# Kernel tuning notes

Hardware: AMD Instinct MI355X
Metric: run time of the kernel (lower is better)

## Reference

```python
import jax, jax.numpy as jnp
import numpy as np

LEAK = 0.01  # torch LeakyReLU default negative_slope

def lrelu(x):
    return jnp.where(x >= 0, x, LEAK * x)

def edge_conv(x, src, dst, ea, W1, b1, W2, b2):
    # message: cat(x_i=target, x_j=source, edge_attr) -> Linear -> LeakyReLU -> Linear
    m = jnp.concatenate([x[dst], x[src], ea], axis=1)          # [E, 2F+Fe]
    h = lrelu(m @ W1 + b1) @ W2 + b2                            # [E, H]
    n = x.shape[0]
    agg = jnp.full((n, h.shape[1]), jnp.inf, h.dtype).at[dst].min(h)  # scatter-min at target
    return jnp.where(jnp.isfinite(agg), agg, jnp.zeros_like(agg))     # empty nodes -> 0


def setup_inputs() -> dict:
    key = jax.random.key(0)
    ks = jax.random.split(key, 20)
    B, N, E = 4, 20000, 640000
    NF, AD, EF, H = 2, 1, 1, 8
    inp = {
        "node_features": jax.random.randint(ks[0], (B, N, NF), 0, 10, dtype=jnp.int32),
        "actions": jax.random.normal(ks[1], (B, N), dtype=jnp.float32),
        "edge_index": jax.random.randint(ks[2], (B, 2, E), 0, N, dtype=jnp.int64),
        "edge_features": jax.random.normal(ks[3], (B, E, EF), dtype=jnp.float32),
    }
    d0 = NF + AD  # 3
    def lin(k, fin, fout):
        s = 1.0 / np.sqrt(fin)
        k1, k2 = jax.random.split(k)
        return (jax.random.uniform(k1, (fin, fout), jnp.float32, -s, s),
                jax.random.uniform(k2, (fout,), jnp.float32, -s, s))
    inp["c1_W1"], inp["c1_b1"] = lin(ks[4], 2 * d0 + EF, H)
    inp["c1_W2"], inp["c1_b2"] = lin(ks[5], H, H)
    inp["c2_W1"], inp["c2_b1"] = lin(ks[6], 2 * H + 1, H)
    inp["c2_W2"], inp["c2_b2"] = lin(ks[7], H, H)
    inp["c3_W1"], inp["c3_b1"] = lin(ks[8], 2 * H + 1, H)
    inp["c3_W2"], inp["c3_b2"] = lin(ks[9], H, H)
    inp["lin_W"], inp["lin_b"] = lin(ks[10], d0 + H, 1)
    return inp


def reference(node_features, actions, edge_index, edge_features,
              c1_W1, c1_b1, c1_W2, c1_b2,
              c2_W1, c2_b1, c2_W2, c2_b2,
              c3_W1, c3_b1, c3_W2, c3_b2,
              lin_W, lin_b):
    # x = int(node_features) concat actions  -> float
    x0 = jnp.concatenate([node_features.astype(jnp.int32).astype(jnp.float32),
                          actions[..., None]], axis=-1)  # [B,N,3]

    def per_graph(x0g, eig, eag):
        src, dst = eig[0], eig[1]  # flow source_to_target: x_j=src, x_i=dst
        h = lrelu(edge_conv(x0g, src, dst, eag, c1_W1, c1_b1, c1_W2, c1_b2))
        h = lrelu(edge_conv(h, src, dst, eag, c2_W1, c2_b1, c2_W2, c2_b2))
        h = lrelu(edge_conv(h, src, dst, eag, c3_W1, c3_b1, c3_W2, c3_b2))
        xc = jnp.concatenate([x0g, h], axis=1)  # [N, 3+8]
        return jnp.sum(xc, axis=0)              # sum-pool over nodes

    pooled = jax.vmap(per_graph)(x0, edge_index, edge_features)  # [B, 11]
    return pooled @ lin_W + lin_b  # [B, 1]
```

## Files before the change

### kernel.cpp

```cpp
#include <hip/hip_runtime.h>
#include <hip/hip_cooperative_groups.h>

#define LEAK 0.01f
#define BS 128
#define PCHUNK 4096
#define PT 512
#define CT 512
#define MAXNB 256
#define CPGMAX 256
#define BARSTRIDE 64

__device__ __forceinline__ float lrelu(float v) {
    return v >= 0.f ? v : LEAK * v;
}

__device__ __forceinline__ unsigned int fmin_encode(float x) {
    unsigned int u = __float_as_uint(x);
    return (u & 0x80000000u) ? ~u : (u | 0x80000000u);
}
__device__ __forceinline__ float fmin_decode(unsigned int k) {
    unsigned int u = (k & 0x80000000u) ? (k ^ 0x80000000u) : ~k;
    return __uint_as_float(u);
}

__device__ __forceinline__ unsigned int bf16_rne(float f) {
    unsigned int u = __float_as_uint(f);
    return (u + 0x7FFFu + ((u >> 16) & 1u)) >> 16;
}

__device__ __forceinline__ void block_add(float c, float* dst) {
    __shared__ float wsum[8];
#pragma unroll
    for (int off = 32; off > 0; off >>= 1) c += __shfl_down(c, off, 64);
    int lane = threadIdx.x & 63;
    int wave = threadIdx.x >> 6;
    if (lane == 0) wsum[wave] = c;
    __syncthreads();
    if (threadIdx.x == 0) {
        float s = 0.f;
        int nw = blockDim.x >> 6;
        for (int w = 0; w < nw; ++w) s += wsum[w];
        atomicAdd(dst, s);
    }
}

__device__ __forceinline__ void graph_barrier(int* bar, int target) {
    __syncthreads();
    if (threadIdx.x == 0) {
        __threadfence();
        __hip_atomic_fetch_add(bar, 1, __ATOMIC_RELEASE, __HIP_MEMORY_SCOPE_AGENT);
        while (__hip_atomic_load(bar, __ATOMIC_RELAXED, __HIP_MEMORY_SCOPE_AGENT) <
               target)
            __builtin_amdgcn_s_sleep(2);
        __threadfence();
    }
    __syncthreads();
}


__device__ __forceinline__ void init_body(
    const int* __restrict__ nf, const float* __restrict__ act,
    const float* __restrict__ W1, const float* __restrict__ b1,
    const float* __restrict__ lw, const float* __restrict__ lb,
    float* __restrict__ a1, unsigned short* __restrict__ a2,
    float* __restrict__ out, int N, int b, int ib) {
    int t = threadIdx.x;
    int n = ib * PT + t;
    float c = 0.f;
    if (n < N) {
        size_t i = (size_t)b * N + n;
        float x0 = (float)nf[i * 2 + 0];
        float x1 = (float)nf[i * 2 + 1];
        float x2 = act[i];
        float v1[8], v2[8];
#pragma unroll
        for (int j = 0; j < 8; ++j) {
            v1[j] = b1[j] + x0 * W1[0 * 8 + j] + x1 * W1[1 * 8 + j] + x2 * W1[2 * 8 + j];
            v2[j] =         x0 * W1[3 * 8 + j] + x1 * W1[4 * 8 + j] + x2 * W1[5 * 8 + j];
        }
        float4* o1 = (float4*)(a1 + i * 8);
        o1[0] = make_float4(v1[0], v1[1], v1[2], v1[3]);
        o1[1] = make_float4(v1[4], v1[5], v1[6], v1[7]);
        unsigned int w[4];
#pragma unroll
        for (int q = 0; q < 4; ++q)
            w[q] = bf16_rne(v2[2 * q]) | (bf16_rne(v2[2 * q + 1]) << 16);
        *(int4*)(a2 + i * 8) = make_int4(w[0], w[1], w[2], w[3]);
        c = x0 * lw[0] + x1 * lw[1] + x2 * lw[2];
        if (n == 0) c += lb[0];
    }
    block_add(c, &out[b]);
}

__device__ __forceinline__ void part_body(
    const int* __restrict__ ei, const float* __restrict__ ea,
    int2* __restrict__ pairs, int* __restrict__ ofs,
    int E, int NB, int CPG, int b, int c,
    int* __restrict__ lc, int* __restrict__ lofs, int* __restrict__ ts) {
    int t = threadIdx.x;
    for (int i = t; i < NB; i += PT) lc[i] = 0;
    __syncthreads();

    int e0 = c * PCHUNK;
    int end = min(e0 + PCHUNK, E);
    const int* srow = ei + (size_t)b * 2 * E;
    const int* drow = srow + E;

    int pk[PCHUNK / PT];
#pragma unroll
    for (int j = 0; j < PCHUNK / PT; ++j) {
        int e = e0 + j * PT + t;
        int p = -1;
        if (e < end) {
            int d = drow[e];
            int bin = d >> 7;
            int r = atomicAdd(&lc[bin], 1);
            p = bin | ((d & 127) << 10) | (r << 17);
        }
        pk[j] = p;
    }
    __syncthreads();

    int v = (t < NB) ? lc[t] : 0;
    ts[t] = v;
    __syncthreads();
    int incl = v;
    for (int off = 1; off < PT; off <<= 1) {
        int add = (t >= off) ? ts[t - off] : 0;
        __syncthreads();
        incl += add;
        ts[t] = incl;
        __syncthreads();
    }
    if (t < NB) lofs[t] = incl - v;
    if (t == PT - 1) lofs[NB] = incl;
    __syncthreads();

    for (int i = t; i <= NB; i += PT) {
        int w = lofs[i];
        ofs[((size_t)b * (NB + 1) + i) * CPG + c] = w;
        if (i < NB) lc[i] = w;
    }
    __syncthreads();

    size_t pbase = (size_t)b * E + e0;
#pragma unroll
    for (int j = 0; j < PCHUNK / PT; ++j) {
        int e = e0 + j * PT + t;
        if (e < end) {
            int p = pk[j];
            int bin = p & 1023;
            int dl = (p >> 10) & 127;
            int r = p >> 17;
            int pos = lc[bin] + r;
            pairs[pbase + pos] =
                make_int2(srow[e] | (dl << 16), __float_as_int(ea[(size_t)b * E + e]));
        }
    }
}

__device__ __forceinline__ void compact_body(
    const int* __restrict__ ofs, const int2* __restrict__ pairs,
    int2* __restrict__ cpairs, int* __restrict__ gofs,
    int E, int NB, int CPG, int b, int bin,
    int* __restrict__ rs, int* __restrict__ re, int* __restrict__ cs,
    int* __restrict__ redsum) {
    int t = threadIdx.x;
    const int* ofb = ofs + ((size_t)b * (NB + 1) + bin) * CPG;
    if (t == 0) *redsum = 0;
    for (int i = t; i < CPGMAX; i += CT) cs[i] = 0;
    __syncthreads();

    int lsum = 0;
    for (int c = t; c < CPG; c += CT) {
        int s = ofb[c];
        int len = ofb[CPG + c] - s;
        rs[c] = s;
        re[c] = len;
        cs[c] = len;
        lsum += s;
    }
#pragma unroll
    for (int off = 32; off > 0; off >>= 1) lsum += __shfl_down(lsum, off, 64);
    if ((t & 63) == 0 && lsum != 0) atomicAdd(redsum, lsum);
    __syncthreads();

    for (int off = 1; off < CPGMAX; off <<= 1) {
        int a = 0;
        if (t < CPGMAX) { a = cs[t]; if (t >= off) a += cs[t - off]; }
        __syncthreads();
        if (t < CPGMAX) cs[t] = a;
        __syncthreads();
    }
    int base = *redsum;
    int* gofsb = gofs + (size_t)b * (NB + 1);
    if (t == 0) {
        gofsb[bin] = base;
        if (bin == NB - 1) gofsb[NB] = base + cs[CPG - 1];
    }

    const int2* pg = pairs + (size_t)b * E;
    int2* cp = cpairs + (size_t)b * E;
    int w = t >> 6, lane = t & 63;
    const int nw = CT >> 6;
    for (int c = w; c < CPG; c += nw) {
        int len = re[c];
        int src = c * PCHUNK + rs[c];
        int dst = base + cs[c] - len;
        for (int i = lane; i < len; i += 64)
            cp[dst + i] = pg[src + i];
    }
}

__device__ __forceinline__ void conv_edge_compute(
    const float* we, const float* bb, const float* __restrict__ W2,
    int2 p, int4 raw, const float* __restrict__ a1s,
    unsigned int* __restrict__ acc) {
    int dl = (p.x >> 16) & 127;
    float eav = __int_as_float(p.y);
    unsigned int wq[4] = {(unsigned int)raw.x, (unsigned int)raw.y,
                          (unsigned int)raw.z, (unsigned int)raw.w};
    float a2v[8];
#pragma unroll
    for (int q = 0; q < 4; ++q) {
        a2v[2 * q]     = __uint_as_float(wq[q] << 16);
        a2v[2 * q + 1] = __uint_as_float(wq[q] & 0xFFFF0000u);
    }
    float h1[8];
#pragma unroll
    for (int j = 0; j < 8; ++j) {
        h1[j] = a1s[dl * 9 + j] + a2v[j];
        h1[j] = fmaf(eav, we[j], h1[j]);
        h1[j] = lrelu(h1[j]);
    }
    float h2[8];
#pragma unroll
    for (int j = 0; j < 8; ++j) h2[j] = bb[j];
#pragma unroll
    for (int kk = 0; kk < 8; ++kk) {
        float hk = h1[kk];
#pragma unroll
        for (int j = 0; j < 8; ++j) h2[j] = fmaf(hk, W2[kk * 8 + j], h2[j]);
    }
#pragma unroll
    for (int j = 0; j < 8; ++j)
        atomicMin(&acc[dl * 9 + j], fmin_encode(h2[j]));
}

__device__ __forceinline__ void conv_edges_dense(
    const unsigned short* __restrict__ a2g, const float* we, const float* bb,
    const float* __restrict__ W2, const int2* __restrict__ cpg,
    int start, int end,
    const float* __restrict__ a1s, unsigned int* __restrict__ acc) {
    for (int k = start + (int)threadIdx.x; k < end; k += CT) {
        int2 p = cpg[k];
        int4 v = *(const int4*)(a2g + (size_t)(p.x & 0xFFFF) * 8);
        conv_edge_compute(we, bb, W2, p, v, a1s, acc);
    }
}

__device__ __forceinline__ void conv_mid_body(
    const float* __restrict__ a1, const unsigned short* __restrict__ a2,
    const float* __restrict__ w1e, const float* __restrict__ W2,
    const float* __restrict__ b2,
    const float* __restrict__ nW1, const float* __restrict__ nb1,
    const int* __restrict__ gofs, const int2* __restrict__ cpairs,
    float* __restrict__ na1, unsigned short* __restrict__ na2,
    int N, int NB, int E, int b, int bin,
    float* __restrict__ a1s, unsigned int* __restrict__ acc) {
    int n0 = bin << 7;
    int nCnt = min(BS, N - n0);
    int t = threadIdx.x;
    size_t node0 = (size_t)b * N + n0;

    for (int i = t; i < nCnt * 8; i += CT)
        a1s[(i >> 3) * 9 + (i & 7)] = a1[node0 * 8 + i];
    for (int i = t; i < BS * 9; i += CT) acc[i] = 0xFFFFFFFFu;
    float we[8], bb[8];
#pragma unroll
    for (int j = 0; j < 8; ++j) { we[j] = w1e[j]; bb[j] = b2[j]; }
    const int* gofsb = gofs + (size_t)b * (NB + 1);
    int start = gofsb[bin];
    int end = gofsb[bin + 1];
    __syncthreads();

    conv_edges_dense(a2 + (size_t)b * N * 8, we, bb, W2,
                     cpairs + (size_t)b * E, start, end, a1s, acc);
    __syncthreads();

    for (int i = t; i < nCnt * 8; i += CT) {
        float v = fmin_decode(acc[(i >> 3) * 9 + (i & 7)]);
        unsigned int u = __float_as_uint(v);
        if ((u & 0x7F800000u) == 0x7F800000u) v = 0.f;
        a1s[(i >> 3) * 9 + (i & 7)] = lrelu(v);
    }
    __syncthreads();

    for (int nh = t; nh < nCnt * 2; nh += CT) {
        int node = nh >> 1, half = nh & 1;
        float h[8];
#pragma unroll
        for (int j = 0; j < 8; ++j) h[j] = a1s[node * 9 + j];
        float v[8];
#pragma unroll
        for (int j = 0; j < 8; ++j) v[j] = half ? 0.f : nb1[j];
        const float* Wbase = nW1 + (half ? 64 : 0);
#pragma unroll
        for (int k = 0; k < 8; ++k) {
            float hk = h[k];
#pragma unroll
            for (int j = 0; j < 8; ++j) v[j] = fmaf(hk, Wbase[k * 8 + j], v[j]);
        }
        if (half) {
            unsigned int w[4];
#pragma unroll
            for (int q = 0; q < 4; ++q)
                w[q] = bf16_rne(v[2 * q]) | (bf16_rne(v[2 * q + 1]) << 16);
            *(int4*)(na2 + (node0 + node) * 8) = make_int4(w[0], w[1], w[2], w[3]);
        } else {
            float4* o = (float4*)(na1 + (node0 + node) * 8);
            o[0] = make_float4(v[0], v[1], v[2], v[3]);
            o[1] = make_float4(v[4], v[5], v[6], v[7]);
        }
    }
    __syncthreads();
}

__device__ __forceinline__ void conv_final_body(
    const float* __restrict__ a1, const unsigned short* __restrict__ a2,
    const float* __restrict__ w1e, const float* __restrict__ W2,
    const float* __restrict__ b2, const float* __restrict__ lw,
    const int* __restrict__ gofs, const int2* __restrict__ cpairs,
    float* __restrict__ out, int N, int NB, int E, int b, int bin,
    float* __restrict__ a1s, unsigned int* __restrict__ acc) {
    int n0 = bin << 7;
    int nCnt = min(BS, N - n0);
    int t = threadIdx.x;
    size_t node0 = (size_t)b * N + n0;

    for (int i = t; i < nCnt * 8; i += CT)
        a1s[(i >> 3) * 9 + (i & 7)] = a1[node0 * 8 + i];
    for (int i = t; i < BS * 9; i += CT) acc[i] = 0xFFFFFFFFu;
    float we[8], bb[8];
#pragma unroll
    for (int j = 0; j < 8; ++j) { we[j] = w1e[j]; bb[j] = b2[j]; }
    const int* gofsb = gofs + (size_t)b * (NB + 1);
    int start = gofsb[bin];
    int end = gofsb[bin + 1];
    __syncthreads();

    conv_edges_dense(a2 + (size_t)b * N * 8, we, bb, W2,
                     cpairs + (size_t)b * E, start, end, a1s, acc);
    __syncthreads();

    float c = 0.f;
    if (t < nCnt) {
#pragma unroll
        for (int j = 0; j < 8; ++j) {
            float v = fmin_decode(acc[t * 9 + j]);
            unsigned int u = __float_as_uint(v);
            if ((u & 0x7F800000u) == 0x7F800000u) v = 0.f;
            c = fmaf(lrelu(v), lw[3 + j], c);
        }
    }
    __syncthreads();
    block_add(c, &out[b]);
}


struct MegaParams {
    const int* ei; const float* ea;
    int2* pairs; int* ofs;
    int2* cpairs; int* gofs;
    const int* nf; const float* act;
    const float* W11; const float* b11; const float* W21; const float* b21;
    const float* W12; const float* b12; const float* W22; const float* b22;
    const float* W13; const float* b13; const float* W23; const float* b23;
    const float* lw; const float* lb;
    float* a1A; unsigned short* a2A; float* a1B; unsigned short* a2B;
    float* out;
    int* bar;
    int E, N, NB, CPG, initBlocks;
};

__global__ __launch_bounds__(512, 8) void mega_kernel(MegaParams P) {
    __shared__ int lc[MAXNB];
    __shared__ int lofs[MAXNB + 1];
    __shared__ int ts[PT];
    __shared__ float a1s[BS * 9];
    __shared__ unsigned int acc[BS * 9];
    __shared__ int rs[CPGMAX];
    __shared__ int re[CPGMAX];
    __shared__ int cs[CPGMAX];
    __shared__ int redsum;
    int b = blockIdx.y, bx = blockIdx.x;
    int* bar = P.bar + b * BARSTRIDE;
    const int gx = gridDim.x;

    if (bx < P.CPG)
        part_body(P.ei, P.ea, P.pairs, P.ofs, P.E, P.NB, P.CPG, b, bx, lc, lofs, ts);
    else if (bx - P.CPG < P.initBlocks)
        init_body(P.nf, P.act, P.W11, P.b11, P.lw, P.lb, P.a1A, P.a2A, P.out,
                  P.N, b, bx - P.CPG);
    graph_barrier(bar, gx);
    if (bx < P.NB)
        compact_body(P.ofs, P.pairs, P.cpairs, P.gofs, P.E, P.NB, P.CPG,
                     b, bx, rs, re, cs, &redsum);
    graph_barrier(bar, gx * 2);
    if (bx < P.NB)
        conv_mid_body(P.a1A, P.a2A, P.W11 + 6 * 8, P.W21, P.b21, P.W12, P.b12,
                      P.gofs, P.cpairs, P.a1B, P.a2B, P.N, P.NB, P.E,
                      b, bx, a1s, acc);
    graph_barrier(bar, gx * 3);
    if (bx < P.NB)
        conv_mid_body(P.a1B, P.a2B, P.W12 + 16 * 8, P.W22, P.b22, P.W13, P.b13,
                      P.gofs, P.cpairs, P.a1A, P.a2A, P.N, P.NB, P.E,
                      b, bx, a1s, acc);
    graph_barrier(bar, gx * 4);
    if (bx < P.NB)
        conv_final_body(P.a1A, P.a2A, P.W13 + 16 * 8, P.W23, P.b23, P.lw,
                        P.gofs, P.cpairs, P.out, P.N, P.NB, P.E,
                        b, bx, a1s, acc);
}


__global__ __launch_bounds__(PT) void part_init_kernel(
    const int* __restrict__ ei, const float* __restrict__ ea,
    int2* __restrict__ pairs, int* __restrict__ ofs,
    const int* __restrict__ nf, const float* __restrict__ act,
    const float* __restrict__ W1, const float* __restrict__ b1,
    const float* __restrict__ lw, const float* __restrict__ lb,
    float* __restrict__ a1, unsigned short* __restrict__ a2,
    float* __restrict__ out, int E, int N, int NB, int CPG) {
    __shared__ int lc[MAXNB];
    __shared__ int lofs[MAXNB + 1];
    __shared__ int ts[PT];
    int b = blockIdx.y;
    if (blockIdx.x >= CPG) {
        init_body(nf, act, W1, b1, lw, lb, a1, a2, out, N, b, blockIdx.x - CPG);
        return;
    }
    part_body(ei, ea, pairs, ofs, E, NB, CPG, b, blockIdx.x, lc, lofs, ts);
}

__global__ __launch_bounds__(CT) void compact_kernel(
    const int* __restrict__ ofs, const int2* __restrict__ pairs,
    int2* __restrict__ cpairs, int* __restrict__ gofs,
    int E, int NB, int CPG) {
    __shared__ int rs[CPGMAX];
    __shared__ int re[CPGMAX];
    __shared__ int cs[CPGMAX];
    __shared__ int redsum;
    compact_body(ofs, pairs, cpairs, gofs, E, NB, CPG,
                 blockIdx.y, blockIdx.x, rs, re, cs, &redsum);
}

__global__ __launch_bounds__(CT) void conv_mid_kernel(
    const float* __restrict__ a1, const unsigned short* __restrict__ a2,
    const float* __restrict__ w1e, const float* __restrict__ W2,
    const float* __restrict__ b2,
    const float* __restrict__ nW1, const float* __restrict__ nb1,
    const int* __restrict__ gofs, const int2* __restrict__ cpairs,
    float* __restrict__ na1, unsigned short* __restrict__ na2,
    int N, int NB, int E) {
    __shared__ float a1s[BS * 9];
    __shared__ unsigned int acc[BS * 9];
    conv_mid_body(a1, a2, w1e, W2, b2, nW1, nb1, gofs, cpairs, na1, na2,
                  N, NB, E, blockIdx.y, blockIdx.x, a1s, acc);
}

__global__ __launch_bounds__(CT) void conv_final_kernel(
    const float* __restrict__ a1, const unsigned short* __restrict__ a2,
    const float* __restrict__ w1e, const float* __restrict__ W2,
    const float* __restrict__ b2, const float* __restrict__ lw,
    const int* __restrict__ gofs, const int2* __restrict__ cpairs,
    float* __restrict__ out, int N, int NB, int E) {
    __shared__ float a1s[BS * 9];
    __shared__ unsigned int acc[BS * 9];
    conv_final_body(a1, a2, w1e, W2, b2, lw, gofs, cpairs, out,
                    N, NB, E, blockIdx.y, blockIdx.x, a1s, acc);
}


__global__ __launch_bounds__(256) void node_init_kernel(
    const int* __restrict__ nf, const float* __restrict__ act,
    float* __restrict__ x0, int BN) {
    int tid = blockIdx.x * blockDim.x + threadIdx.x;
    if (tid >= BN) return;
    x0[tid * 3 + 0] = (float)nf[tid * 2 + 0];
    x0[tid * 3 + 1] = (float)nf[tid * 2 + 1];
    x0[tid * 3 + 2] = act[tid];
}

template <int D>
__global__ __launch_bounds__(256) void edge_conv_kernel(
    const float* __restrict__ x, const int* __restrict__ ei,
    const float* __restrict__ ea,
    const float* __restrict__ W1, const float* __restrict__ b1,
    const float* __restrict__ W2, const float* __restrict__ b2,
    unsigned int* __restrict__ agg, int E, int N, int B) {
    int tid = blockIdx.x * blockDim.x + threadIdx.x;
    if (tid >= B * E) return;
    int b = tid / E;
    int e = tid - b * E;
    const int* eb = ei + (size_t)b * 2 * E;
    int s = eb[e];
    int d = eb[E + e];
    const float* xi = x + ((size_t)b * N + d) * D;
    const float* xj = x + ((size_t)b * N + s) * D;
    constexpr int M = 2 * D + 1;
    float m[M];
#pragma unroll
    for (int k = 0; k < D; ++k) { m[k] = xi[k]; m[D + k] = xj[k]; }
    m[2 * D] = ea[(size_t)b * E + e];
    float h1[8];
#pragma unroll
    for (int j = 0; j < 8; ++j) h1[j] = b1[j];
#pragma unroll
    for (int k = 0; k < M; ++k) {
        float mk = m[k];
#pragma unroll
        for (int j = 0; j < 8; ++j) h1[j] = fmaf(mk, W1[k * 8 + j], h1[j]);
    }
#pragma unroll
    for (int j = 0; j < 8; ++j) h1[j] = lrelu(h1[j]);
    float h2[8];
#pragma unroll
    for (int j = 0; j < 8; ++j) h2[j] = b2[j];
#pragma unroll
    for (int k = 0; k < 8; ++k) {
        float hk = h1[k];
#pragma unroll
        for (int j = 0; j < 8; ++j) h2[j] = fmaf(hk, W2[k * 8 + j], h2[j]);
    }
    unsigned int* ag = agg + ((size_t)b * N + d) * 8;
#pragma unroll
    for (int j = 0; j < 8; ++j) atomicMin(&ag[j], fmin_encode(h2[j]));
}

__global__ __launch_bounds__(256) void finalize_kernel(
    unsigned int* __restrict__ agg, int total) {
    int tid = blockIdx.x * blockDim.x + threadIdx.x;
    if (tid >= total) return;
    float v = fmin_decode(agg[tid]);
    unsigned int u = __float_as_uint(v);
    if ((u & 0x7F800000u) == 0x7F800000u) v = 0.f;
    ((float*)agg)[tid] = lrelu(v);
}

__global__ __launch_bounds__(256) void pool_kernel(
    const float* __restrict__ x0, const float* __restrict__ h,
    const float* __restrict__ lw, const float* __restrict__ lb,
    float* __restrict__ out, int N) {
    int b = blockIdx.y;
    int n = blockIdx.x * blockDim.x + threadIdx.x;
    float c = 0.f;
    if (n < N) {
        const float* x = x0 + ((size_t)b * N + n) * 3;
        const float* hh = h + ((size_t)b * N + n) * 8;
        c = x[0] * lw[0] + x[1] * lw[1] + x[2] * lw[2];
#pragma unroll
        for (int k = 0; k < 8; ++k) c = fmaf(hh[k], lw[3 + k], c);
        if (n == 0) c += lb[0];
    }
    block_add(c, &out[b]);
}


static inline size_t align256(size_t x) { return (x + 255) & ~(size_t)255; }

extern "C" void kernel_launch(void* const* d_in, const int* in_sizes, int n_in,
                              void* d_out, int out_size, void* d_ws, size_t ws_size,
                              hipStream_t stream) {
    const int B = 4;
    const int N = in_sizes[1] / B;
    const int E = in_sizes[2] / (2 * B);

    const int*   nf  = (const int*)d_in[0];
    const float* act = (const float*)d_in[1];
    const int*   ei  = (const int*)d_in[2];
    const float* ea  = (const float*)d_in[3];
    const float* c1_W1 = (const float*)d_in[4];
    const float* c1_b1 = (const float*)d_in[5];
    const float* c1_W2 = (const float*)d_in[6];
    const float* c1_b2 = (const float*)d_in[7];
    const float* c2_W1 = (const float*)d_in[8];
    const float* c2_b1 = (const float*)d_in[9];
    const float* c2_W2 = (const float*)d_in[10];
    const float* c2_b2 = (const float*)d_in[11];
    const float* c3_W1 = (const float*)d_in[12];
    const float* c3_b1 = (const float*)d_in[13];
    const float* c3_W2 = (const float*)d_in[14];
    const float* c3_b2 = (const float*)d_in[15];
    const float* lw    = (const float*)d_in[16];
    const float* lb    = (const float*)d_in[17];
    float* out = (float*)d_out;

    const int BN = B * N;
    const int BE = B * E;
    const int NB = (N + BS - 1) / BS;
    const int CPG = (E + PCHUNK - 1) / PCHUNK;
    const int initBlocks = (N + PT - 1) / PT;

    char* ws = (char*)d_ws;
    size_t off = 0;
    float* a1A = (float*)(ws + off);           off += align256((size_t)BN * 8 * 4);
    float* a1B = (float*)(ws + off);           off += align256((size_t)BN * 8 * 4);
    unsigned short* a2A = (unsigned short*)(ws + off); off += align256((size_t)BN * 8 * 2);
    unsigned short* a2B = (unsigned short*)(ws + off); off += align256((size_t)BN * 8 * 2);
    int* ofs    = (int*)(ws + off);    off += align256((size_t)B * (NB + 1) * CPG * 4);
    int2* pairs = (int2*)(ws + off);   off += align256((size_t)BE * 8);
    int2* cpairs = (int2*)(ws + off);  off += align256((size_t)BE * 8);
    int* gofs   = (int*)(ws + off);    off += align256((size_t)B * (NB + 1) * 4);
    float* x0   = (float*)(ws + off);  off += align256((size_t)BN * 3 * 4);
    int* bar    = (int*)(ws + off);    off += align256((size_t)B * BARSTRIDE * 4);
    const bool useFast = (off <= ws_size) && (NB <= MAXNB) && (CPG <= CPGMAX) &&
                         (N <= 32768);

    hipMemsetAsync(out, 0, (size_t)B * sizeof(float), stream);

    if (useFast) {
        const int gx = (CPG + initBlocks > NB) ? (CPG + initBlocks) : NB;

        int dev = 0;
        hipGetDevice(&dev);
        int numCU = 0;
        hipDeviceGetAttribute(&numCU, hipDeviceAttributeMultiprocessorCount, dev);
        int occ = 0;
        hipOccupancyMaxActiveBlocksPerMultiprocessor(&occ, mega_kernel, 512, 0);
        const bool canCoop = (occ > 0) && ((size_t)occ * (size_t)numCU >=
                                           (size_t)gx * (size_t)B);

        if (canCoop) {
            hipMemsetAsync(bar, 0, (size_t)B * BARSTRIDE * sizeof(int), stream);
            MegaParams P;
            P.ei = ei; P.ea = ea; P.pairs = pairs; P.ofs = ofs;
            P.cpairs = cpairs; P.gofs = gofs;
            P.nf = nf; P.act = act;
            P.W11 = c1_W1; P.b11 = c1_b1; P.W21 = c1_W2; P.b21 = c1_b2;
            P.W12 = c2_W1; P.b12 = c2_b1; P.W22 = c2_W2; P.b22 = c2_b2;
            P.W13 = c3_W1; P.b13 = c3_b1; P.W23 = c3_W2; P.b23 = c3_b2;
            P.lw = lw; P.lb = lb;
            P.a1A = a1A; P.a2A = a2A; P.a1B = a1B; P.a2B = a2B;
            P.out = out; P.bar = bar;
            P.E = E; P.N = N; P.NB = NB; P.CPG = CPG; P.initBlocks = initBlocks;
            void* args[] = {&P};
            hipLaunchCooperativeKernel((void*)mega_kernel, dim3(gx, B),
                                       dim3(512), args, 0, stream);
        } else {
            dim3 pgrid(CPG + initBlocks, B);
            dim3 cgrid(NB, B);
            part_init_kernel<<<pgrid, PT, 0, stream>>>(
                ei, ea, pairs, ofs, nf, act, c1_W1, c1_b1, lw, lb,
                a1A, a2A, out, E, N, NB, CPG);
            compact_kernel<<<cgrid, CT, 0, stream>>>(
                ofs, pairs, cpairs, gofs, E, NB, CPG);
            conv_mid_kernel<<<cgrid, CT, 0, stream>>>(
                a1A, a2A, c1_W1 + 6 * 8, c1_W2, c1_b2, c2_W1, c2_b1,
                gofs, cpairs, a1B, a2B, N, NB, E);
            conv_mid_kernel<<<cgrid, CT, 0, stream>>>(
                a1B, a2B, c2_W1 + 16 * 8, c2_W2, c2_b2, c3_W1, c3_b1,
                gofs, cpairs, a1A, a2A, N, NB, E);
            conv_final_kernel<<<cgrid, CT, 0, stream>>>(
                a1A, a2A, c3_W1 + 16 * 8, c3_W2, c3_b2, lw,
                gofs, cpairs, out, N, NB, E);
        }
    } else {
        const int egrid = (BE + 255) / 256;
        const int aggTotal = BN * 8;
        const int agrid = (aggTotal + 255) / 256;
        const size_t aggBytes = (size_t)aggTotal * 4;
        unsigned int* uA = (unsigned int*)a1A;
        unsigned int* uB = (unsigned int*)a1B;

        node_init_kernel<<<(BN + 255) / 256, 256, 0, stream>>>(nf, act, x0, BN);

        hipMemsetAsync(uA, 0xFF, aggBytes, stream);
        edge_conv_kernel<3><<<egrid, 256, 0, stream>>>(
            x0, ei, ea, c1_W1, c1_b1, c1_W2, c1_b2, uA, E, N, B);
        finalize_kernel<<<agrid, 256, 0, stream>>>(uA, aggTotal);

        hipMemsetAsync(uB, 0xFF, aggBytes, stream);
        edge_conv_kernel<8><<<egrid, 256, 0, stream>>>(
            (const float*)uA, ei, ea, c2_W1, c2_b1, c2_W2, c2_b2, uB, E, N, B);
        finalize_kernel<<<agrid, 256, 0, stream>>>(uB, aggTotal);

        hipMemsetAsync(uA, 0xFF, aggBytes, stream);
        edge_conv_kernel<8><<<egrid, 256, 0, stream>>>(
            (const float*)uB, ei, ea, c3_W1, c3_b1, c3_W2, c3_b2, uA, E, N, B);
        finalize_kernel<<<agrid, 256, 0, stream>>>(uA, aggTotal);

        dim3 plgrid((N + 255) / 256, B);
        pool_kernel<<<plgrid, 256, 0, stream>>>(x0, (const float*)uA, lw, lb, out, N);
    }
}
```

Baseline: 199.1 us.

## Replace partition+compact with count/scatter passes writing directly to sorted edge array

The per-chunk partition plus separate compaction pass is replaced by a count pass and a scatter pass. The scatter pass computes global bin offsets from all chunk counts and writes edges straight into the final compacted array, removing one full round trip of the intermediate pairs buffer. It also unrolls the dense edge loop four-wide to batch gathers, and lengthens the barrier spin sleep. The cost is that each scatter block rereads the edge indices and scans all chunk counts, and the longer sleep may add barrier latency.

```diff
diff --git a/kernel.cpp b/kernel.cpp
--- a/kernel.cpp
+++ b/kernel.cpp
@@ -51,7 +51,7 @@
         __hip_atomic_fetch_add(bar, 1, __ATOMIC_RELEASE, __HIP_MEMORY_SCOPE_AGENT);
         while (__hip_atomic_load(bar, __ATOMIC_RELAXED, __HIP_MEMORY_SCOPE_AGENT) <
                target)
-            __builtin_amdgcn_s_sleep(2);
+            __builtin_amdgcn_s_sleep(16);
         __threadfence();
     }
     __syncthreads();
@@ -92,17 +92,30 @@
     block_add(c, &out[b]);
 }
 
-__device__ __forceinline__ void part_body(
+__device__ __forceinline__ void count_body(
+    const int* __restrict__ ei, int* __restrict__ cnt,
+    int E, int NB, int CPG, int b, int c, int* __restrict__ lc) {
+    int t = threadIdx.x;
+    for (int i = t; i < NB; i += PT) lc[i] = 0;
+    __syncthreads();
+    int e0 = c * PCHUNK, end = min(e0 + PCHUNK, E);
+    const int* drow = ei + (size_t)b * 2 * E + E;
+    for (int e = e0 + t; e < end; e += PT)
+        atomicAdd(&lc[drow[e] >> 7], 1);
+    __syncthreads();
+    int* crow = cnt + ((size_t)b * CPG + c) * NB;
+    for (int i = t; i < NB; i += PT) crow[i] = lc[i];
+}
+
+__device__ __forceinline__ void scatter_body(
     const int* __restrict__ ei, const float* __restrict__ ea,
-    int2* __restrict__ pairs, int* __restrict__ ofs,
-    int E, int NB, int CPG, int b, int c,
+    const int* __restrict__ cnt, int2* __restrict__ cpairs,
+    int* __restrict__ gofs, int E, int NB, int CPG, int b, int c,
     int* __restrict__ lc, int* __restrict__ lofs, int* __restrict__ ts) {
     int t = threadIdx.x;
     for (int i = t; i < NB; i += PT) lc[i] = 0;
     __syncthreads();
-
-    int e0 = c * PCHUNK;
-    int end = min(e0 + PCHUNK, E);
+    int e0 = c * PCHUNK, end = min(e0 + PCHUNK, E);
     const int* srow = ei + (size_t)b * 2 * E;
     const int* drow = srow + E;
 
@@ -119,9 +132,17 @@
         }
         pk[j] = p;
     }
-    __syncthreads();
-
-    int v = (t < NB) ? lc[t] : 0;
+
+    const int* cb = cnt + (size_t)b * CPG * NB;
+    int partial = 0, full = 0;
+    if (t < NB) {
+        for (int c2 = 0; c2 < CPG; ++c2) {
+            int v = cb[(size_t)c2 * NB + t];
+            full += v;
+            if (c2 < c) partial += v;
+        }
+    }
+    int v = (t < NB) ? full : 0;
     ts[t] = v;
     __syncthreads();
     int incl = v;
@@ -132,18 +153,14 @@
         ts[t] = incl;
         __syncthreads();
     }
-    if (t < NB) lofs[t] = incl - v;
-    if (t == PT - 1) lofs[NB] = incl;
-    __syncthreads();
-
-    for (int i = t; i <= NB; i += PT) {
-        int w = lofs[i];
-        ofs[((size_t)b * (NB + 1) + i) * CPG + c] = w;
-        if (i < NB) lc[i] = w;
-    }
-    __syncthreads();
-
-    size_t pbase = (size_t)b * E + e0;
+    if (t < NB) lofs[t] = (incl - v) + partial;
+    if (c == 0) {
+        if (t < NB) gofs[(size_t)b * (NB + 1) + t] = incl - v;
+        if (t == PT - 1) gofs[(size_t)b * (NB + 1) + NB] = incl;
+    }
+    __syncthreads();
+
+    int2* cp = cpairs + (size_t)b * E;
 #pragma unroll
     for (int j = 0; j < PCHUNK / PT; ++j) {
         int e = e0 + j * PT + t;
@@ -152,63 +169,9 @@
             int bin = p & 1023;
             int dl = (p >> 10) & 127;
             int r = p >> 17;
-            int pos = lc[bin] + r;
-            pairs[pbase + pos] =
+            cp[lofs[bin] + r] =
                 make_int2(srow[e] | (dl << 16), __float_as_int(ea[(size_t)b * E + e]));
         }
-    }
-}
-
-__device__ __forceinline__ void compact_body(
-    const int* __restrict__ ofs, const int2* __restrict__ pairs,
-    int2* __restrict__ cpairs, int* __restrict__ gofs,
-    int E, int NB, int CPG, int b, int bin,
-    int* __restrict__ rs, int* __restrict__ re, int* __restrict__ cs,
-    int* __restrict__ redsum) {
-    int t = threadIdx.x;
-    const int* ofb = ofs + ((size_t)b * (NB + 1) + bin) * CPG;
-    if (t == 0) *redsum = 0;
-    for (int i = t; i < CPGMAX; i += CT) cs[i] = 0;
-    __syncthreads();
-
-    int lsum = 0;
-    for (int c = t; c < CPG; c += CT) {
-        int s = ofb[c];
-        int len = ofb[CPG + c] - s;
-        rs[c] = s;
-        re[c] = len;
-        cs[c] = len;
-        lsum += s;
-    }
-#pragma unroll
-    for (int off = 32; off > 0; off >>= 1) lsum += __shfl_down(lsum, off, 64);
-    if ((t & 63) == 0 && lsum != 0) atomicAdd(redsum, lsum);
-    __syncthreads();
-
-    for (int off = 1; off < CPGMAX; off <<= 1) {
-        int a = 0;
-        if (t < CPGMAX) { a = cs[t]; if (t >= off) a += cs[t - off]; }
-        __syncthreads();
-        if (t < CPGMAX) cs[t] = a;
-        __syncthreads();
-    }
-    int base = *redsum;
-    int* gofsb = gofs + (size_t)b * (NB + 1);
-    if (t == 0) {
-        gofsb[bin] = base;
-        if (bin == NB - 1) gofsb[NB] = base + cs[CPG - 1];
-    }
-
-    const int2* pg = pairs + (size_t)b * E;
-    int2* cp = cpairs + (size_t)b * E;
-    int w = t >> 6, lane = t & 63;
-    const int nw = CT >> 6;
-    for (int c = w; c < CPG; c += nw) {
-        int len = re[c];
-        int src = c * PCHUNK + rs[c];
-        int dst = base + cs[c] - len;
-        for (int i = lane; i < len; i += 64)
-            cp[dst + i] = pg[src + i];
     }
 }
 
@@ -252,8 +215,24 @@
     const float* __restrict__ W2, const int2* __restrict__ cpg,
     int start, int end,
     const float* __restrict__ a1s, unsigned int* __restrict__ acc) {
-    for (int k = start + (int)threadIdx.x; k < end; k += CT) {
-        int2 p = cpg[k];
+    int t = threadIdx.x;
+    int k = start + t * 4;
+    for (; k + 3 < end; k += CT * 4) {
+        int2 p0 = cpg[k];
+        int2 p1 = cpg[k + 1];
+        int2 p2 = cpg[k + 2];
+        int2 p3 = cpg[k + 3];
+        int4 v0 = *(const int4*)(a2g + (size_t)(p0.x & 0xFFFF) * 8);
+        int4 v1 = *(const int4*)(a2g + (size_t)(p1.x & 0xFFFF) * 8);
+        int4 v2 = *(const int4*)(a2g + (size_t)(p2.x & 0xFFFF) * 8);
+        int4 v3 = *(const int4*)(a2g + (size_t)(p3.x & 0xFFFF) * 8);
+        conv_edge_compute(we, bb, W2, p0, v0, a1s, acc);
+        conv_edge_compute(we, bb, W2, p1, v1, a1s, acc);
+        conv_edge_compute(we, bb, W2, p2, v2, a1s, acc);
+        conv_edge_compute(we, bb, W2, p3, v3, a1s, acc);
+    }
+    for (int e = k; e < end && e < k + 4; ++e) {
+        int2 p = cpg[e];
         int4 v = *(const int4*)(a2g + (size_t)(p.x & 0xFFFF) * 8);
         conv_edge_compute(we, bb, W2, p, v, a1s, acc);
     }
@@ -370,8 +349,7 @@
 
 struct MegaParams {
     const int* ei; const float* ea;
-    int2* pairs; int* ofs;
-    int2* cpairs; int* gofs;
+    int* cnt; int2* cpairs; int* gofs;
     const int* nf; const float* act;
     const float* W11; const float* b11; const float* W21; const float* b21;
     const float* W12; const float* b12; const float* W22; const float* b22;
@@ -389,23 +367,19 @@
     __shared__ int ts[PT];
     __shared__ float a1s[BS * 9];
     __shared__ unsigned int acc[BS * 9];
-    __shared__ int rs[CPGMAX];
-    __shared__ int re[CPGMAX];
-    __shared__ int cs[CPGMAX];
-    __shared__ int redsum;
     int b = blockIdx.y, bx = blockIdx.x;
     int* bar = P.bar + b * BARSTRIDE;
     const int gx = gridDim.x;
 
     if (bx < P.CPG)
-        part_body(P.ei, P.ea, P.pairs, P.ofs, P.E, P.NB, P.CPG, b, bx, lc, lofs, ts);
+        count_body(P.ei, P.cnt, P.E, P.NB, P.CPG, b, bx, lc);
     else if (bx - P.CPG < P.initBlocks)
         init_body(P.nf, P.act, P.W11, P.b11, P.lw, P.lb, P.a1A, P.a2A, P.out,
                   P.N, b, bx - P.CPG);
     graph_barrier(bar, gx);
-    if (bx < P.NB)
-        compact_body(P.ofs, P.pairs, P.cpairs, P.gofs, P.E, P.NB, P.CPG,
-                     b, bx, rs, re, cs, &redsum);
+    if (bx < P.CPG)
+        scatter_body(P.ei, P.ea, P.cnt, P.cpairs, P.gofs, P.E, P.NB, P.CPG,
+                     b, bx, lc, lofs, ts);
     graph_barrier(bar, gx * 2);
     if (bx < P.NB)
         conv_mid_body(P.a1A, P.a2A, P.W11 + 6 * 8, P.W21, P.b21, P.W12, P.b12,
@@ -424,35 +398,31 @@
 }
 
 
-__global__ __launch_bounds__(PT) void part_init_kernel(
-    const int* __restrict__ ei, const float* __restrict__ ea,
-    int2* __restrict__ pairs, int* __restrict__ ofs,
+__global__ __launch_bounds__(PT) void count_init_kernel(
+    const int* __restrict__ ei, int* __restrict__ cnt,
     const int* __restrict__ nf, const float* __restrict__ act,
     const float* __restrict__ W1, const float* __restrict__ b1,
     const float* __restrict__ lw, const float* __restrict__ lb,
     float* __restrict__ a1, unsigned short* __restrict__ a2,
     float* __restrict__ out, int E, int N, int NB, int CPG) {
     __shared__ int lc[MAXNB];
-    __shared__ int lofs[MAXNB + 1];
-    __shared__ int ts[PT];
     int b = blockIdx.y;
     if (blockIdx.x >= CPG) {
         init_body(nf, act, W1, b1, lw, lb, a1, a2, out, N, b, blockIdx.x - CPG);
         return;
     }
-    part_body(ei, ea, pairs, ofs, E, NB, CPG, b, blockIdx.x, lc, lofs, ts);
-}
-
-__global__ __launch_bounds__(CT) void compact_kernel(
-    const int* __restrict__ ofs, const int2* __restrict__ pairs,
-    int2* __restrict__ cpairs, int* __restrict__ gofs,
-    int E, int NB, int CPG) {
-    __shared__ int rs[CPGMAX];
-    __shared__ int re[CPGMAX];
-    __shared__ int cs[CPGMAX];
-    __shared__ int redsum;
-    compact_body(ofs, pairs, cpairs, gofs, E, NB, CPG,
-                 blockIdx.y, blockIdx.x, rs, re, cs, &redsum);
+    count_body(ei, cnt, E, NB, CPG, b, blockIdx.x, lc);
+}
+
+__global__ __launch_bounds__(PT) void scatter_kernel(
+    const int* __restrict__ ei, const float* __restrict__ ea,
+    const int* __restrict__ cnt, int2* __restrict__ cpairs,
+    int* __restrict__ gofs, int E, int NB, int CPG) {
+    __shared__ int lc[MAXNB];
+    __shared__ int lofs[MAXNB + 1];
+    __shared__ int ts[PT];
+    scatter_body(ei, ea, cnt, cpairs, gofs, E, NB, CPG,
+                 blockIdx.y, blockIdx.x, lc, lofs, ts);
 }
 
 __global__ __launch_bounds__(CT) void conv_mid_kernel(
@@ -608,8 +578,7 @@
     float* a1B = (float*)(ws + off);           off += align256((size_t)BN * 8 * 4);
     unsigned short* a2A = (unsigned short*)(ws + off); off += align256((size_t)BN * 8 * 2);
     unsigned short* a2B = (unsigned short*)(ws + off); off += align256((size_t)BN * 8 * 2);
-    int* ofs    = (int*)(ws + off);    off += align256((size_t)B * (NB + 1) * CPG * 4);
-    int2* pairs = (int2*)(ws + off);   off += align256((size_t)BE * 8);
+    int* cnt    = (int*)(ws + off);    off += align256((size_t)B * CPG * NB * 4);
     int2* cpairs = (int2*)(ws + off);  off += align256((size_t)BE * 8);
     int* gofs   = (int*)(ws + off);    off += align256((size_t)B * (NB + 1) * 4);
     float* x0   = (float*)(ws + off);  off += align256((size_t)BN * 3 * 4);
@@ -634,8 +603,7 @@
         if (canCoop) {
             hipMemsetAsync(bar, 0, (size_t)B * BARSTRIDE * sizeof(int), stream);
             MegaParams P;
-            P.ei = ei; P.ea = ea; P.pairs = pairs; P.ofs = ofs;
-            P.cpairs = cpairs; P.gofs = gofs;
+            P.ei = ei; P.ea = ea; P.cnt = cnt; P.cpairs = cpairs; P.gofs = gofs;
             P.nf = nf; P.act = act;
             P.W11 = c1_W1; P.b11 = c1_b1; P.W21 = c1_W2; P.b21 = c1_b2;
             P.W12 = c2_W1; P.b12 = c2_b1; P.W22 = c2_W2; P.b22 = c2_b2;
@@ -649,12 +617,13 @@
                                        dim3(512), args, 0, stream);
         } else {
             dim3 pgrid(CPG + initBlocks, B);
+            dim3 sgrid(CPG, B);
             dim3 cgrid(NB, B);
-            part_init_kernel<<<pgrid, PT, 0, stream>>>(
-                ei, ea, pairs, ofs, nf, act, c1_W1, c1_b1, lw, lb,
-                a1A, a2A, out, E, N, NB, CPG);
-            compact_kernel<<<cgrid, CT, 0, stream>>>(
-                ofs, pairs, cpairs, gofs, E, NB, CPG);
+            count_init_kernel<<<pgrid, PT, 0, stream>>>(
+                ei, cnt, nf, act, c1_W1, c1_b1, lw, lb, a1A, a2A, out,
+                E, N, NB, CPG);
+            scatter_kernel<<<sgrid, PT, 0, stream>>>(
+                ei, ea, cnt, cpairs, gofs, E, NB, CPG);
             conv_mid_kernel<<<cgrid, CT, 0, stream>>>(
                 a1A, a2A, c1_W1 + 6 * 8, c1_W2, c1_b2, c2_W1, c2_b1,
                 gofs, cpairs, a1B, a2B, N, NB, E);
```

Result: slower. 234.0 us (+17.5%).
